# Kernel tuning notes

Hardware: AMD Instinct MI355X
Metric: run time of the kernel (lower is better)

The kernel has to match this reference:

```python
import jax, jax.numpy as jnp
import numpy as np

# Module hyperparameters (from init_kwargs)
H, F = 8, 32            # num_heads, attention_filters
RY, RX = 3, 3           # spatial_radius
PH, PW = 2 * RY + 1, 2 * RX + 1
S = PH * PW             # patch_size = 49
HF = H * F


def setup_inputs() -> dict:
    key = jax.random.key(0)
    ks = jax.random.split(key, 6)
    B, Y, X, C = 4, 64, 64, 256
    x = jax.random.normal(ks[0], (B, Y, X, C), jnp.float32)
    # 1x1 conv kernels == dense matrices over the channel dim (no bias)
    Wq = jax.random.normal(ks[1], (C, HF), jnp.float32) / np.sqrt(C)
    Wk = jax.random.normal(ks[2], (C, HF), jnp.float32) / np.sqrt(C)
    Wv = jax.random.normal(ks[3], (C, HF), jnp.float32) / np.sqrt(C)
    Wo = jax.random.normal(ks[4], (HF, C), jnp.float32) / np.sqrt(HF)
    pos_emb = jax.random.normal(ks[5], (S, HF), jnp.float32) * 0.02
    return {"x": x, "Wq": Wq, "Wk": Wk, "Wv": Wv, "Wo": Wo, "pos_emb": pos_emb}


def reference(x, Wq, Wk, Wv, Wo, pos_emb):
    B, Y, X, C = x.shape
    dtype = x.dtype
    # 1x1 conv projections
    Q = x @ Wq                       # (B,Y,X,HF)
    K = x @ Wk
    V = x @ Wv
    # clipped patch centers (borders reuse interior patches)
    cy = jnp.clip(jnp.arange(Y), RY, Y - RY - 1)   # (Y,)
    cx = jnp.clip(jnp.arange(X), RX, X - RX - 1)   # (X,)
    # query relative-position indices within its patch
    qy = jnp.arange(Y) - cy + RY
    qx = jnp.arange(X) - cx + RX
    qidx = qy[:, None] * PW + qx[None, :]          # (Y,X) in [0,S)
    Q = Q + pos_emb[qidx]                          # add query pos embedding (HF)
    Q = Q.reshape(B, Y, X, H, F)
    K = K.reshape(B, Y, X, H, F)
    V = V.reshape(B, Y, X, H, F)
    cy_g, cx_g = jnp.meshgrid(cy, cx, indexing="ij")  # (Y,X)
    scale = jnp.asarray(1.0 / np.sqrt(F), dtype)
    NEG = jnp.asarray(-1e9, dtype)
    m = jnp.full((B, Y, X, H, 1), NEG, dtype)      # running max
    l = jnp.zeros((B, Y, X, H, 1), dtype)          # running sum-exp
    acc = jnp.zeros((B, Y, X, H, F), dtype)        # running value accumulator
    dy_vec = np.arange(-RY, RY + 1)                # within-chunk offsets ('col' mode)
    for dx in range(-RX, RX + 1):                  # chunk loop over columns (7 chunks)
        ny = jnp.clip(cy_g[None, :, :] + dy_vec[:, None, None], 0, Y - 1)  # (PH,Y,X)
        nx = jnp.clip(cx_g[None, :, :] + dx, 0, X - 1)                     # (1,Y,X)
        nx = jnp.broadcast_to(nx, ny.shape)
        sidx = (dy_vec + RY) * PW + (dx + RX)      # (PH,) relative-pos indices
        # gather neighbor K/V: (B,PH,Y,X,H,F)
        Kc = K[:, ny, nx] + pos_emb[sidx].reshape(PH, 1, 1, H, F)
        Vc = V[:, ny, nx]
        sc = jnp.einsum("byxhf,bsyxhf->byxhs", Q, Kc) * scale  # (B,Y,X,H,PH)
        new_m = jnp.maximum(m, sc.max(axis=-1, keepdims=True))
        alpha = jnp.exp(m - new_m)
        p = jnp.exp(sc - new_m)
        l = l * alpha + p.sum(axis=-1, keepdims=True)
        acc = acc * alpha + jnp.einsum("byxhs,bsyxhf->byxhf", p, Vc)
        m = new_m
    out = (acc / (l + 1e-8)).reshape(B, Y, X, HF) @ Wo
    return out
```

## Files before the change

kernel.cpp:

```cpp
#include <hip/hip_runtime.h>
#include <hip/hip_bf16.h>

static constexpr int NPOS = 4 * 64 * 64;
static constexpr int CD   = 256;
#define QSCALE (0.17677669529663687f * 1.4426950408889634f)

typedef __attribute__((ext_vector_type(8))) short bf16x8;
typedef __attribute__((ext_vector_type(4))) float f32x4;

__device__ __forceinline__ float bflo(unsigned int u) { return __uint_as_float(u << 16); }
__device__ __forceinline__ float bfhi(unsigned int u) { return __uint_as_float(u & 0xffff0000u); }

__device__ __forceinline__ unsigned short bfbits(float f) {
    union { __hip_bfloat16 h; unsigned short u; } cv;
    cv.h = __float2bfloat16(f);
    return cv.u;
}
__device__ __forceinline__ unsigned int packbf2(float lo, float hi) {
    union { __hip_bfloat162 h; unsigned int u; } cv;
    cv.h.x = __float2bfloat16(lo);
    cv.h.y = __float2bfloat16(hi);
    return cv.u;
}
__device__ __forceinline__ uint4 pack8(float4 a, float4 b) {
    uint4 u;
    u.x = packbf2(a.x, a.y); u.y = packbf2(a.z, a.w);
    u.z = packbf2(b.x, b.y); u.w = packbf2(b.z, b.w);
    return u;
}
template<int CTRL>
__device__ __forceinline__ float dpp_mov(float v) {
    return __int_as_float(
        __builtin_amdgcn_update_dpp(0, __float_as_int(v), CTRL, 0xF, 0xF, true));
}
template<int IMM>
__device__ __forceinline__ float swz(float v) {
    return __int_as_float(__builtin_amdgcn_ds_swizzle(__float_as_int(v), IMM));
}
__device__ __forceinline__ void async16(void* lds, const void* g) {
    __builtin_amdgcn_global_load_lds(
        (const __attribute__((address_space(1))) unsigned int*)g,
        (__attribute__((address_space(3))) unsigned int*)lds, 16, 0, 0);
}

__global__ __launch_bounds__(256) void convertx_kernel(
    const float* __restrict__ x, unsigned short* __restrict__ xb)
{
    int t = blockIdx.x * 256 + threadIdx.x;
    const float4* s = (const float4*)x + (size_t)t * 2;
    float4 a = s[0], b = s[1];
    ((uint4*)xb)[t] = pack8(a, b);
}

__global__ __launch_bounds__(256) void convert1_kernel(
    const float* __restrict__ Wq, const float* __restrict__ Wk,
    const float* __restrict__ Wv, const float* __restrict__ Wo,
    const float* __restrict__ pe,
    __hip_bfloat16* __restrict__ Wfrag,
    __hip_bfloat16* __restrict__ pebf,
    __hip_bfloat16* __restrict__ Wofrag)
{
    int t = blockIdx.x * 256 + threadIdx.x;
    if (t < 24576) {
        int L = t & 63, ng = (t >> 6) & 7, s = (t >> 9) & 7, T = t >> 12;
        int mat = T >> 1;
        const float* src = (mat == 0) ? Wq : (mat == 1) ? Wk : Wv;
        int ncol  = (T & 1) * 128 + ng * 16 + (L & 15);
        int kbase = s * 32 + (L >> 4) * 8;
        __hip_bfloat16* dst = Wfrag + ((size_t)((T * 8 + s) * 8 + ng) * 64 + L) * 8;
#pragma unroll
        for (int j = 0; j < 8; ++j)
            dst[j] = __float2bfloat16(src[(kbase + j) * 256 + ncol]);
    } else if (t < 26624) {
        int u = t - 24576;
        int L = u & 63, Tn = (u >> 6) & 3, h = u >> 8;
        int s = Tn * 16 + (L & 15);
        int kbase = (L >> 4) * 8;
        __hip_bfloat16* dst = pebf + ((size_t)((h * 4 + Tn) * 64 + L)) * 8;
#pragma unroll
        for (int j = 0; j < 8; ++j) {
            float v = (s < 49) ? pe[s * 256 + h * 32 + kbase + j] * QSCALE : 0.f;
            dst[j] = __float2bfloat16(v);
        }
    } else if (t < 34816) {
        int u = t - 26624;
        int L = u & 63, ng = (u >> 6) & 7, s = (u >> 9) & 7, T = (u >> 12) & 1;
        int ncol  = T * 128 + ng * 16 + (L & 15);
        int kbase = s * 32 + (L >> 4) * 8;
        __hip_bfloat16* dst = Wofrag + ((size_t)((T * 8 + s) * 8 + ng) * 64 + L) * 8;
#pragma unroll
        for (int j = 0; j < 8; ++j)
            dst[j] = __float2bfloat16(Wo[(kbase + j) * 256 + ncol]);
    }
}

__global__ __launch_bounds__(256, 4) void qkv_mfma(
    const unsigned short* __restrict__ xb,
    const __hip_bfloat16* __restrict__ Wfrag,
    const float* __restrict__ pe,
    unsigned short* __restrict__ QA,
    unsigned short* __restrict__ Kd,
    unsigned short* __restrict__ Vt)
{
    __shared__ __align__(16) short As[2][64 * 32];
    const int t = threadIdx.x;
    const int rowbase = blockIdx.x * 64;
    const int g = blockIdx.y;
    const int L = t & 63;
    const int wave = t >> 6;
    const int quad = L >> 4, lrow = L & 15;
    const int T = g * 2 + (wave >> 1);
    const int ngb = (wave & 1) * 4;

    f32x4 acc[4][4];
#pragma unroll
    for (int i = 0; i < 4; ++i)
#pragma unroll
        for (int j = 0; j < 4; ++j) acc[i][j] = (f32x4){0.f, 0.f, 0.f, 0.f};

    const unsigned short* xs = xb + (size_t)(rowbase + (t >> 2)) * CD + (t & 3) * 8;
    short* d0 = &As[0][t * 8];
    short* d1 = &As[1][t * 8];

    async16(d0, xs);
    __syncthreads();

#pragma unroll
    for (int s = 0; s < 8; ++s) {
        if (s < 7) async16((s & 1) ? d0 : d1, xs + (s + 1) * 32);
        bf16x8 bfr[4];
#pragma unroll
        for (int j = 0; j < 4; ++j)
            bfr[j] = *(const bf16x8*)(Wfrag +
                      ((size_t)((T * 8 + s) * 8 + ngb + j) * 64 + L) * 8);
        const short* Ab = As[s & 1];
#pragma unroll
        for (int i = 0; i < 4; ++i) {
            bf16x8 af = *(const bf16x8*)(Ab + (i * 16 + lrow) * 32 + quad * 8);
#pragma unroll
            for (int j = 0; j < 4; ++j)
                acc[i][j] = __builtin_amdgcn_mfma_f32_16x16x32_bf16(af, bfr[j], acc[i][j], 0, 0, 0);
        }
        __syncthreads();
    }

#pragma unroll
    for (int i = 0; i < 4; ++i) {
#pragma unroll
        for (int r = 0; r < 4; ++r) {
            int row = rowbase + i * 16 + quad * 4 + r;
            if (g == 0) {
                int yy = (row >> 6) & 63, xx = row & 63;
                int cy = min(max(yy, 3), 60), cx = min(max(xx, 3), 60);
                int qidx = (yy - cy + 3) * 7 + (xx - cx + 3);
#pragma unroll
                for (int j = 0; j < 4; ++j) {
                    int c = wave * 64 + j * 16 + lrow;
                    QA[(size_t)row * CD + c] = bfbits(acc[i][j][r] + pe[qidx * 256 + c]);
                }
            } else if (g == 1) {
#pragma unroll
                for (int j = 0; j < 4; ++j) {
                    int c = wave * 64 + j * 16 + lrow;
                    Kd[(size_t)row * CD + c] = bfbits(acc[i][j][r] * QSCALE);
                }
            } else {
#pragma unroll
                for (int j = 0; j < 4; ++j) {
                    int c = wave * 64 + j * 16 + lrow;
                    Vt[(size_t)c * 16384 + row + 3] = bfbits(acc[i][j][r]);
                }
            }
        }
    }
}

__global__ __launch_bounds__(256) void attn_mfma(
    unsigned short* QA,
    const unsigned short* __restrict__ Kd,
    const unsigned short* __restrict__ Vt,
    const __hip_bfloat16* __restrict__ pebf)
{
    __shared__ float qpes[4][16 * 64];
    __shared__ __align__(16) unsigned short ps[4][16 * 40];
    const int t = threadIdx.x, w = t >> 6, L = t & 63;
    const int lrow = L & 15, quad = L >> 4;
    const int id = blockIdx.x * 4 + w;
    const int tile = id >> 3, h = id & 7;
    const int pos0 = tile * 16;
    const int x0 = pos0 & 63;
    const int yy = (pos0 >> 6) & 63, bb = pos0 >> 12;
    const int cy = min(max(yy, 3), 60);

    int cxr[4];
#pragma unroll
    for (int r = 0; r < 4; ++r)
        cxr[r] = min(max(x0 + quad * 4 + r, 3), 60) - x0;

    const int kc0 = min(max(x0 - 3 + lrow, 0), 63);
    const int kc1 = min(max(x0 + 13 + lrow, 0), 63);

    const bf16x8 qa = *(const bf16x8*)(QA + (size_t)(pos0 + lrow) * 256 + h * 32 + quad * 8);

    float* qp = qpes[w];
    const f32x4 zero = {0.f, 0.f, 0.f, 0.f};
#pragma unroll
    for (int Tn = 0; Tn < 4; ++Tn) {
        bf16x8 bp = *(const bf16x8*)(pebf + ((size_t)((h * 4 + Tn) * 64 + L)) * 8);
        f32x4 c = __builtin_amdgcn_mfma_f32_16x16x32_bf16(qa, bp, zero, 0, 0, 0);
#pragma unroll
        for (int r = 0; r < 4; ++r)
            qp[(quad * 4 + r) * 64 + Tn * 16 + lrow] = c[r];
    }
    __builtin_amdgcn_s_waitcnt(0xc07f);

    float lacc[4] = {0.f, 0.f, 0.f, 0.f};
    f32x4 o0 = zero, o1 = zero;
    unsigned short* pw = ps[w];
    int rowpos = bb * 4096 + (cy - 3) * 64;

    for (int dy = 0; dy < 7; ++dy, rowpos += 64) {
        const bf16x8 bk0 = *(const bf16x8*)(Kd + (size_t)(rowpos + kc0) * 256 + h * 32 + quad * 8);
        const bf16x8 bk1 = *(const bf16x8*)(Kd + (size_t)(rowpos + kc1) * 256 + h * 32 + quad * 8);
        f32x4 sc0 = __builtin_amdgcn_mfma_f32_16x16x32_bf16(qa, bk0, zero, 0, 0, 0);
        f32x4 sc1 = __builtin_amdgcn_mfma_f32_16x16x32_bf16(qa, bk1, zero, 0, 0, 0);
        const int dy7 = dy * 7;
#pragma unroll
        for (int r = 0; r < 4; ++r) {
            const int i = quad * 4 + r;
            {
                int dx3 = lrow - cxr[r];
                float qpe = qp[i * 64 + dy7 + min(max(dx3, 0), 6)];
                float e = exp2f(sc0[r] + qpe);
                float p = ((unsigned)dx3 <= 6u) ? e : 0.f;
                lacc[r] += p;
                pw[i * 40 + lrow] = bfbits(p);
            }
            {
                int dx3 = 16 + lrow - cxr[r];
                float qpe = qp[i * 64 + dy7 + min(max(dx3, 0), 6)];
                float e = exp2f(sc1[r] + qpe);
                float p = ((unsigned)dx3 <= 6u) ? e : 0.f;
                lacc[r] += p;
                pw[i * 40 + 16 + lrow] = bfbits(p);
            }
        }
        __builtin_amdgcn_s_waitcnt(0xc07f);
        const bf16x8 pa = *(const bf16x8*)(pw + lrow * 40 + quad * 8);
        const bf16x8 bv0 = *(const bf16x8*)(Vt + (size_t)(h * 32 + lrow) * 16384 + rowpos + x0 + quad * 8);
        const bf16x8 bv1 = *(const bf16x8*)(Vt + (size_t)(h * 32 + 16 + lrow) * 16384 + rowpos + x0 + quad * 8);
        o0 = __builtin_amdgcn_mfma_f32_16x16x32_bf16(pa, bv0, o0, 0, 0, 0);
        o1 = __builtin_amdgcn_mfma_f32_16x16x32_bf16(pa, bv1, o1, 0, 0, 0);
    }

#pragma unroll
    for (int r = 0; r < 4; ++r) {
        float v = lacc[r];
        v += dpp_mov<0xB1>(v);
        v += dpp_mov<0x4E>(v);
        v += swz<0x101F>(v);
        v += swz<0x201F>(v);
        const float inv = 1.f / (v + 1e-8f);
        const int row = pos0 + quad * 4 + r;
        QA[(size_t)row * 256 + h * 32 + lrow]      = bfbits(o0[r] * inv);
        QA[(size_t)row * 256 + h * 32 + 16 + lrow] = bfbits(o1[r] * inv);
    }
}

__global__ __launch_bounds__(256, 4) void oproj_mfma(
    const unsigned short* __restrict__ A,
    const __hip_bfloat16* __restrict__ Wofrag,
    float* __restrict__ out)
{
    __shared__ __align__(16) short As[2][32 * 32];
    const int t = threadIdx.x;
    const int rowbase = blockIdx.x * 32;
    const int L = t & 63;
    const int wave = t >> 6;
    const int quad = L >> 4, lrow = L & 15;
    const int T = wave >> 1;
    const int ngb = (wave & 1) * 4;

    f32x4 acc[2][4];
#pragma unroll
    for (int i = 0; i < 2; ++i)
#pragma unroll
        for (int j = 0; j < 4; ++j) acc[i][j] = (f32x4){0.f, 0.f, 0.f, 0.f};

    const unsigned short* asrc = A + (size_t)(rowbase + (t >> 2)) * CD + (t & 3) * 8;
    short* d0 = &As[0][t * 8];
    short* d1 = &As[1][t * 8];

    if (t < 128) async16(d0, asrc);
    __syncthreads();

#pragma unroll
    for (int s = 0; s < 8; ++s) {
        if (s < 7 && t < 128) async16((s & 1) ? d0 : d1, asrc + (s + 1) * 32);
        bf16x8 bfr[4];
#pragma unroll
        for (int j = 0; j < 4; ++j)
            bfr[j] = *(const bf16x8*)(Wofrag +
                      ((size_t)((T * 8 + s) * 8 + ngb + j) * 64 + L) * 8);
        const short* Ab = As[s & 1];
#pragma unroll
        for (int i = 0; i < 2; ++i) {
            bf16x8 af = *(const bf16x8*)(Ab + (i * 16 + lrow) * 32 + quad * 8);
#pragma unroll
            for (int j = 0; j < 4; ++j)
                acc[i][j] = __builtin_amdgcn_mfma_f32_16x16x32_bf16(af, bfr[j], acc[i][j], 0, 0, 0);
        }
        __syncthreads();
    }

#pragma unroll
    for (int i = 0; i < 2; ++i)
#pragma unroll
        for (int r = 0; r < 4; ++r) {
            int row = rowbase + i * 16 + quad * 4 + r;
#pragma unroll
            for (int j = 0; j < 4; ++j) {
                int c = wave * 64 + j * 16 + lrow;
                out[(size_t)row * CD + c] = acc[i][j][r];
            }
        }
}

extern "C" void kernel_launch(void* const* d_in, const int* in_sizes, int n_in,
                              void* d_out, int out_size, void* d_ws, size_t ws_size,
                              hipStream_t stream)
{
    const float* x  = (const float*)d_in[0];
    const float* Wq = (const float*)d_in[1];
    const float* Wk = (const float*)d_in[2];
    const float* Wv = (const float*)d_in[3];
    const float* Wo = (const float*)d_in[4];
    const float* pe = (const float*)d_in[5];
    float* out = (float*)d_out;

    char* ws = (char*)d_ws;
    unsigned short* QA = (unsigned short*)ws;
    unsigned short* Kd = (unsigned short*)(ws + (8u << 20));
    unsigned short* Vt = (unsigned short*)(ws + (16u << 20));
    unsigned short* xb = (unsigned short*)(ws + (24u << 20) + 4096);
    char* fr = ws + (32u << 20) + 8192;
    __hip_bfloat16* Wfrag  = (__hip_bfloat16*)fr;
    __hip_bfloat16* pebf   = (__hip_bfloat16*)(fr + (384u << 10));
    __hip_bfloat16* Wofrag = (__hip_bfloat16*)(fr + (416u << 10));

    convertx_kernel<<<2048, 256, 0, stream>>>(x, xb);
    convert1_kernel<<<136, 256, 0, stream>>>(Wq, Wk, Wv, Wo, pe, Wfrag, pebf, Wofrag);
    qkv_mfma<<<dim3(256, 3), 256, 0, stream>>>(xb, Wfrag, pe, QA, Kd, Vt);
    attn_mfma<<<2048, 256, 0, stream>>>(QA, Kd, Vt, pebf);
    oproj_mfma<<<512, 256, 0, stream>>>(QA, Wofrag, out);
}
```

Baseline: 138.4 us.

## Fuse x bf16 conversion into QKV GEMM, coalesce V transpose, prefetch K/V in attention

Removes the separate x-to-bf16 conversion kernel: the QKV GEMM now loads fp32 x directly, packs it to bf16 and stores it into double-buffered LDS with a register prefetch one step ahead. The V output transpose is staged through shared memory so global writes become contiguous 8-byte stores instead of scattered 2-byte stores. The attention kernel shifts its K/V window to be aligned (offset -8, with +5 added to cxr to compensate) and software-prefetches the next row's K and V fragments. In exchange, qkv_mfma uses a larger LDS allocation, which may limit occupancy, and x is read as fp32 three times, once per grid.y group.

```diff
diff --git a/kernel.cpp b/kernel.cpp
--- a/kernel.cpp
+++ b/kernel.cpp
@@ -7,9 +7,6 @@
 
 typedef __attribute__((ext_vector_type(8))) short bf16x8;
 typedef __attribute__((ext_vector_type(4))) float f32x4;
-
-__device__ __forceinline__ float bflo(unsigned int u) { return __uint_as_float(u << 16); }
-__device__ __forceinline__ float bfhi(unsigned int u) { return __uint_as_float(u & 0xffff0000u); }
 
 __device__ __forceinline__ unsigned short bfbits(float f) {
     union { __hip_bfloat16 h; unsigned short u; } cv;
@@ -43,16 +40,7 @@
         (__attribute__((address_space(3))) unsigned int*)lds, 16, 0, 0);
 }
 
-__global__ __launch_bounds__(256) void convertx_kernel(
-    const float* __restrict__ x, unsigned short* __restrict__ xb)
-{
-    int t = blockIdx.x * 256 + threadIdx.x;
-    const float4* s = (const float4*)x + (size_t)t * 2;
-    float4 a = s[0], b = s[1];
-    ((uint4*)xb)[t] = pack8(a, b);
-}
-
-__global__ __launch_bounds__(256) void convert1_kernel(
+__global__ __launch_bounds__(256) void convert_kernel(
     const float* __restrict__ Wq, const float* __restrict__ Wk,
     const float* __restrict__ Wv, const float* __restrict__ Wo,
     const float* __restrict__ pe,
@@ -95,14 +83,16 @@
 }
 
 __global__ __launch_bounds__(256, 4) void qkv_mfma(
-    const unsigned short* __restrict__ xb,
+    const float* __restrict__ x,
     const __hip_bfloat16* __restrict__ Wfrag,
     const float* __restrict__ pe,
     unsigned short* __restrict__ QA,
     unsigned short* __restrict__ Kd,
     unsigned short* __restrict__ Vt)
 {
-    __shared__ __align__(16) short As[2][64 * 32];
+    __shared__ __align__(16) unsigned short smem[256 * 68];
+    short* As0 = (short*)smem;
+    short* As1 = As0 + 2048;
     const int t = threadIdx.x;
     const int rowbase = blockIdx.x * 64;
     const int g = blockIdx.y;
@@ -118,22 +108,30 @@
 #pragma unroll
         for (int j = 0; j < 4; ++j) acc[i][j] = (f32x4){0.f, 0.f, 0.f, 0.f};
 
-    const unsigned short* xs = xb + (size_t)(rowbase + (t >> 2)) * CD + (t & 3) * 8;
-    short* d0 = &As[0][t * 8];
-    short* d1 = &As[1][t * 8];
-
-    async16(d0, xs);
+    const float* xsrc = x + (size_t)(rowbase + (t >> 2)) * CD + (t & 3) * 8;
+
+    float4 f0 = ((const float4*)xsrc)[0];
+    float4 f1 = ((const float4*)xsrc)[1];
+    ((uint4*)As0)[t] = pack8(f0, f1);
+    f0 = ((const float4*)(xsrc + 32))[0];
+    f1 = ((const float4*)(xsrc + 32))[1];
     __syncthreads();
 
 #pragma unroll
     for (int s = 0; s < 8; ++s) {
-        if (s < 7) async16((s & 1) ? d0 : d1, xs + (s + 1) * 32);
         bf16x8 bfr[4];
 #pragma unroll
         for (int j = 0; j < 4; ++j)
             bfr[j] = *(const bf16x8*)(Wfrag +
                       ((size_t)((T * 8 + s) * 8 + ngb + j) * 64 + L) * 8);
-        const short* Ab = As[s & 1];
+        if (s < 7) {
+            ((uint4*)((s & 1) ? As0 : As1))[t] = pack8(f0, f1);
+            if (s < 6) {
+                f0 = ((const float4*)(xsrc + (s + 2) * 32))[0];
+                f1 = ((const float4*)(xsrc + (s + 2) * 32))[1];
+            }
+        }
+        const short* Ab = (s & 1) ? As1 : As0;
 #pragma unroll
         for (int i = 0; i < 4; ++i) {
             bf16x8 af = *(const bf16x8*)(Ab + (i * 16 + lrow) * 32 + quad * 8);
@@ -144,12 +142,12 @@
         __syncthreads();
     }
 
-#pragma unroll
-    for (int i = 0; i < 4; ++i) {
-#pragma unroll
-        for (int r = 0; r < 4; ++r) {
-            int row = rowbase + i * 16 + quad * 4 + r;
-            if (g == 0) {
+    if (g == 0) {
+#pragma unroll
+        for (int i = 0; i < 4; ++i)
+#pragma unroll
+            for (int r = 0; r < 4; ++r) {
+                int row = rowbase + i * 16 + quad * 4 + r;
                 int yy = (row >> 6) & 63, xx = row & 63;
                 int cy = min(max(yy, 3), 60), cx = min(max(xx, 3), 60);
                 int qidx = (yy - cy + 3) * 7 + (xx - cx + 3);
@@ -158,19 +156,40 @@
                     int c = wave * 64 + j * 16 + lrow;
                     QA[(size_t)row * CD + c] = bfbits(acc[i][j][r] + pe[qidx * 256 + c]);
                 }
-            } else if (g == 1) {
+            }
+    } else if (g == 1) {
+#pragma unroll
+        for (int i = 0; i < 4; ++i)
+#pragma unroll
+            for (int r = 0; r < 4; ++r) {
+                int row = rowbase + i * 16 + quad * 4 + r;
 #pragma unroll
                 for (int j = 0; j < 4; ++j) {
                     int c = wave * 64 + j * 16 + lrow;
                     Kd[(size_t)row * CD + c] = bfbits(acc[i][j][r] * QSCALE);
                 }
-            } else {
-#pragma unroll
-                for (int j = 0; j < 4; ++j) {
-                    int c = wave * 64 + j * 16 + lrow;
-                    Vt[(size_t)c * 16384 + row + 3] = bfbits(acc[i][j][r]);
-                }
-            }
+            }
+    } else {
+        unsigned short* vt = smem;
+#pragma unroll
+        for (int i = 0; i < 4; ++i)
+#pragma unroll
+            for (int j = 0; j < 4; ++j) {
+                int c = wave * 64 + j * 16 + lrow;
+                int row0 = i * 16 + quad * 4;
+                *(unsigned int*)&vt[c * 68 + row0] =
+                    (unsigned int)bfbits(acc[i][j][0]) | ((unsigned int)bfbits(acc[i][j][1]) << 16);
+                *(unsigned int*)&vt[c * 68 + row0 + 2] =
+                    (unsigned int)bfbits(acc[i][j][2]) | ((unsigned int)bfbits(acc[i][j][3]) << 16);
+            }
+        __syncthreads();
+        const int grp = t >> 4, lig = t & 15;
+        const int row_off = lig * 4;
+#pragma unroll
+        for (int pass = 0; pass < 16; ++pass) {
+            int c = pass * 16 + grp;
+            *(ushort4*)(Vt + (size_t)c * 16384 + rowbase + row_off) =
+                *(const ushort4*)&vt[c * 68 + row_off];
         }
     }
 }
@@ -195,10 +214,10 @@
     int cxr[4];
 #pragma unroll
     for (int r = 0; r < 4; ++r)
-        cxr[r] = min(max(x0 + quad * 4 + r, 3), 60) - x0;
-
-    const int kc0 = min(max(x0 - 3 + lrow, 0), 63);
-    const int kc1 = min(max(x0 + 13 + lrow, 0), 63);
+        cxr[r] = min(max(x0 + quad * 4 + r, 3), 60) - x0 + 5;
+
+    const int kc0 = min(max(x0 - 8 + lrow, 0), 63);
+    const int kc1 = min(max(x0 + 8 + lrow, 0), 63);
 
     const bf16x8 qa = *(const bf16x8*)(QA + (size_t)(pos0 + lrow) * 256 + h * 32 + quad * 8);
 
@@ -219,9 +238,23 @@
     unsigned short* pw = ps[w];
     int rowpos = bb * 4096 + (cy - 3) * 64;
 
-    for (int dy = 0; dy < 7; ++dy, rowpos += 64) {
-        const bf16x8 bk0 = *(const bf16x8*)(Kd + (size_t)(rowpos + kc0) * 256 + h * 32 + quad * 8);
-        const bf16x8 bk1 = *(const bf16x8*)(Kd + (size_t)(rowpos + kc1) * 256 + h * 32 + quad * 8);
+    const size_t koff = h * 32 + quad * 8;
+    const size_t voff0 = (size_t)(h * 32 + lrow) * 16384 + x0 - 8 + quad * 8;
+    const size_t voff1 = (size_t)(h * 32 + 16 + lrow) * 16384 + x0 - 8 + quad * 8;
+    bf16x8 bk0 = *(const bf16x8*)(Kd + (size_t)(rowpos + kc0) * 256 + koff);
+    bf16x8 bk1 = *(const bf16x8*)(Kd + (size_t)(rowpos + kc1) * 256 + koff);
+    bf16x8 bv0 = *(const bf16x8*)(Vt + voff0 + rowpos);
+    bf16x8 bv1 = *(const bf16x8*)(Vt + voff1 + rowpos);
+
+    for (int dy = 0; dy < 7; ++dy) {
+        const int rnext = rowpos + 64;
+        bf16x8 nk0, nk1, nv0, nv1;
+        if (dy < 6) {
+            nk0 = *(const bf16x8*)(Kd + (size_t)(rnext + kc0) * 256 + koff);
+            nk1 = *(const bf16x8*)(Kd + (size_t)(rnext + kc1) * 256 + koff);
+            nv0 = *(const bf16x8*)(Vt + voff0 + rnext);
+            nv1 = *(const bf16x8*)(Vt + voff1 + rnext);
+        }
         f32x4 sc0 = __builtin_amdgcn_mfma_f32_16x16x32_bf16(qa, bk0, zero, 0, 0, 0);
         f32x4 sc1 = __builtin_amdgcn_mfma_f32_16x16x32_bf16(qa, bk1, zero, 0, 0, 0);
         const int dy7 = dy * 7;
@@ -247,10 +280,10 @@
         }
         __builtin_amdgcn_s_waitcnt(0xc07f);
         const bf16x8 pa = *(const bf16x8*)(pw + lrow * 40 + quad * 8);
-        const bf16x8 bv0 = *(const bf16x8*)(Vt + (size_t)(h * 32 + lrow) * 16384 + rowpos + x0 + quad * 8);
-        const bf16x8 bv1 = *(const bf16x8*)(Vt + (size_t)(h * 32 + 16 + lrow) * 16384 + rowpos + x0 + quad * 8);
         o0 = __builtin_amdgcn_mfma_f32_16x16x32_bf16(pa, bv0, o0, 0, 0, 0);
         o1 = __builtin_amdgcn_mfma_f32_16x16x32_bf16(pa, bv1, o1, 0, 0, 0);
+        bk0 = nk0; bk1 = nk1; bv0 = nv0; bv1 = nv1;
+        rowpos = rnext;
     }
 
 #pragma unroll
@@ -342,15 +375,13 @@
     unsigned short* QA = (unsigned short*)ws;
     unsigned short* Kd = (unsigned short*)(ws + (8u << 20));
     unsigned short* Vt = (unsigned short*)(ws + (16u << 20));
-    unsigned short* xb = (unsigned short*)(ws + (24u << 20) + 4096);
-    char* fr = ws + (32u << 20) + 8192;
+    char* fr = ws + (24u << 20) + 4096;
     __hip_bfloat16* Wfrag  = (__hip_bfloat16*)fr;
     __hip_bfloat16* pebf   = (__hip_bfloat16*)(fr + (384u << 10));
     __hip_bfloat16* Wofrag = (__hip_bfloat16*)(fr + (416u << 10));
 
-    convertx_kernel<<<2048, 256, 0, stream>>>(x, xb);
-    convert1_kernel<<<136, 256, 0, stream>>>(Wq, Wk, Wv, Wo, pe, Wfrag, pebf, Wofrag);
-    qkv_mfma<<<dim3(256, 3), 256, 0, stream>>>(xb, Wfrag, pe, QA, Kd, Vt);
+    convert_kernel<<<136, 256, 0, stream>>>(Wq, Wk, Wv, Wo, pe, Wfrag, pebf, Wofrag);
+    qkv_mfma<<<dim3(256, 3), 256, 0, stream>>>(x, Wfrag, pe, QA, Kd, Vt);
     attn_mfma<<<2048, 256, 0, stream>>>(QA, Kd, Vt, pebf);
     oproj_mfma<<<512, 256, 0, stream>>>(QA, Wofrag, out);
 }
```

After: 128.6 us. -7.1%, faster.
